# Performance work log

Hardware: AMD Instinct MI355X
Metric: run time of the kernel (lower is better)

The kernel has to match this reference:

```python
import jax, jax.numpy as jnp
import numpy as np
from jax import lax

B, C_IN, L = 32, 64, 8192
PF = 128


def caudil_conv(x, W, kw, dilation, causal_padding=0):
    """x: (B, C, L); W: (O, kw*C) with layout W[o, c*kw + j] (channel-major).
    Equivalent to the per-timestep sliced-Linear loop: VALID dilated conv."""
    C = x.shape[1]
    if causal_padding:
        x = jnp.pad(x, ((0, 0), (0, 0), (causal_padding, 0)))
    K = W.reshape(-1, C, kw)  # (O, C, kw)
    return lax.conv_general_dilated(
        x, K, window_strides=(1,), padding='VALID', rhs_dilation=(dilation,),
        dimension_numbers=('NCH', 'OIH', 'NCH'))


def setup_inputs() -> dict:
    key = jax.random.key(0)
    ks = jax.random.split(key, 10)
    s = lambda k, shp: (jax.random.normal(k, shp, dtype=jnp.float32) * 0.05)
    return {
        'x': jax.random.normal(ks[0], (B, C_IN, L), dtype=jnp.float32),
        'w7_1': s(ks[1], (6, 3 * C_IN)),
        'w7_3': s(ks[2], (PF, 3 * 6)),
        'w10_1': s(ks[3], (6, 3 * C_IN)),
        'w10_3': s(ks[4], (6, 3 * 6)),
        'w10_5': s(ks[5], (PF, 2 * 6)),
        'w15_1': s(ks[6], (6, 3 * C_IN)),
        'w15_3': s(ks[7], (6, 3 * 6)),
        'w15_5': s(ks[8], (PF, 3 * 6)),
    }


def reference(x, w7_1, w7_3, w10_1, w10_3, w10_5, w15_1, w15_3, w15_5):
    relu = jax.nn.relu
    # branch 7: (3,d1) -> (3,d2)
    m7 = relu(caudil_conv(x, w7_1, 3, 1))
    m7 = relu(caudil_conv(m7, w7_3, 3, 2))
    # branch 10: (3,d1) -> (3,d2) -> (2,d4,pad4)
    m10 = relu(caudil_conv(x, w10_1, 3, 1))
    m10 = relu(caudil_conv(m10, w10_3, 3, 2))
    m10 = relu(caudil_conv(m10, w10_5, 2, 4, causal_padding=4))
    # branch 15: (3,d1) -> (3,d2) -> (3,d4,pad8)
    m15 = relu(caudil_conv(x, w15_1, 3, 1))
    m15 = relu(caudil_conv(m15, w15_3, 3, 2))
    m15 = relu(caudil_conv(m15, w15_5, 3, 4, causal_padding=8))
    return jnp.concatenate([m7, m10, m15], axis=1)  # (B, 3*PF, L-6)
```

## Files before the change

kernel.cpp:

```cpp
#include <hip/hip_runtime.h>

constexpr int Bn   = 32;
constexpr int CIN  = 64;
constexpr int Lx   = 8192;
constexpr int L1   = 8190;
constexpr int LOUT = 8186;
constexpr int NCH  = 384;

constexpr int TB = 256;
constexpr int TT = 256;
constexpr int NTILES = (LOUT + TT - 1) / TT;

constexpr int W7v   = TT + 4;
constexpr int W10Av = TT + 8;
constexpr int W15Av = TT + 12;
constexpr int W10Bv = TT + 4;
constexpr int W15Bv = TT + 8;

__global__ void prep_weights(const float* __restrict__ w7_1,
                             const float* __restrict__ w10_1,
                             const float* __restrict__ w15_1,
                             float* __restrict__ ws) {
    int idx = blockIdx.x * blockDim.x + threadIdx.x;
    if (idx >= 64 * 54) return;
    int ci = idx / 54, r = idx % 54;
    int k = r / 3, j = r % 3;
    const float* src = (k < 6) ? w7_1 : ((k < 12) ? w10_1 : w15_1);
    int kk = (k < 6) ? k : ((k < 12) ? k - 6 : k - 12);
    ws[ci * 64 + r] = src[kk * 192 + ci * 3 + j];
}

__device__ __forceinline__ void store4(float* __restrict__ op, int t,
                                       float a0, float a1, float a2, float a3) {
    a0 = fmaxf(a0, 0.f); a1 = fmaxf(a1, 0.f);
    a2 = fmaxf(a2, 0.f); a3 = fmaxf(a3, 0.f);
    if (t + 3 < LOUT) {
        *(float2*)(op + t)     = make_float2(a0, a1);
        *(float2*)(op + t + 2) = make_float2(a2, a3);
    } else {
        if (t     < LOUT) op[t]     = a0;
        if (t + 1 < LOUT) op[t + 1] = a1;
        if (t + 2 < LOUT) op[t + 2] = a2;
        if (t + 3 < LOUT) op[t + 3] = a3;
    }
}

__global__ __launch_bounds__(TB)
void fused_inception(const float* __restrict__ x,
                     const float* __restrict__ wS1,
                     const float* __restrict__ w7_3,
                     const float* __restrict__ w10_3,
                     const float* __restrict__ w10_5,
                     const float* __restrict__ w15_3,
                     const float* __restrict__ w15_5,
                     float* __restrict__ out) {
    __shared__ float h7  [6 * W7v];
    __shared__ float h10a[6 * W10Av];
    __shared__ float h15a[6 * W15Av];
    __shared__ float h10b[6 * W10Bv];
    __shared__ float h15b[6 * W15Bv];

    const int tid  = threadIdx.x;
    const int tile = blockIdx.x;
    const int b    = blockIdx.y;
    const int t0   = tile * TT;
    const float* xb = x + (size_t)b * CIN * Lx;

    for (int p = tid; p < TT + 12; p += TB) {
        const int s = t0 - 8 + p;
        float acc[18];
        #pragma unroll
        for (int k = 0; k < 18; ++k) acc[k] = 0.f;
        if (s >= 0 && s < L1) {
            const float* xr = xb + s;
            for (int ci = 0; ci < CIN; ++ci) {
                const float x0 = xr[ci * Lx];
                const float x1 = xr[ci * Lx + 1];
                const float x2 = xr[ci * Lx + 2];
                const float* wr = wS1 + ci * 64;
                #pragma unroll
                for (int k = 0; k < 18; ++k) {
                    acc[k] = fmaf(wr[k * 3 + 0], x0, acc[k]);
                    acc[k] = fmaf(wr[k * 3 + 1], x1, acc[k]);
                    acc[k] = fmaf(wr[k * 3 + 2], x2, acc[k]);
                }
            }
            #pragma unroll
            for (int k = 0; k < 18; ++k) acc[k] = fmaxf(acc[k], 0.f);
        }
        if (p >= 8) {
            #pragma unroll
            for (int c = 0; c < 6; ++c) h7[c * W7v + (p - 8)] = acc[c];
        }
        if (p >= 4) {
            #pragma unroll
            for (int c = 0; c < 6; ++c) h10a[c * W10Av + (p - 4)] = acc[6 + c];
        }
        #pragma unroll
        for (int c = 0; c < 6; ++c) h15a[c * W15Av + p] = acc[12 + c];
    }
    __syncthreads();

    for (int p = tid; p < W10Bv; p += TB) {
        const int u = t0 - 4 + p;
        float v[18];
        #pragma unroll
        for (int c = 0; c < 6; ++c)
            #pragma unroll
            for (int j = 0; j < 3; ++j)
                v[c * 3 + j] = h10a[c * W10Av + p + 2 * j];
        #pragma unroll
        for (int k = 0; k < 6; ++k) {
            float a = 0.f;
            #pragma unroll
            for (int r = 0; r < 18; ++r) a = fmaf(w10_3[k * 18 + r], v[r], a);
            h10b[k * W10Bv + p] = (u >= 0) ? fmaxf(a, 0.f) : 0.f;
        }
    }
    for (int p = tid; p < W15Bv; p += TB) {
        const int u = t0 - 8 + p;
        float v[18];
        #pragma unroll
        for (int c = 0; c < 6; ++c)
            #pragma unroll
            for (int j = 0; j < 3; ++j)
                v[c * 3 + j] = h15a[c * W15Av + p + 2 * j];
        #pragma unroll
        for (int k = 0; k < 6; ++k) {
            float a = 0.f;
            #pragma unroll
            for (int r = 0; r < 18; ++r) a = fmaf(w15_3[k * 18 + r], v[r], a);
            h15b[k * W15Bv + p] = (u >= 0) ? fmaxf(a, 0.f) : 0.f;
        }
    }
    __syncthreads();

    const int tq = tid & 63;
    const int wv = tid >> 6;
    const int tt = tq * 4;
    const int tglob = t0 + tt;

    {
        float v[6][8];
        #pragma unroll
        for (int c = 0; c < 6; ++c) {
            float4 A = *(const float4*)&h7[c * W7v + tt];
            float4 Bv = *(const float4*)&h7[c * W7v + tt + 4];
            v[c][0] = A.x; v[c][1] = A.y; v[c][2] = A.z; v[c][3] = A.w;
            v[c][4] = Bv.x; v[c][5] = Bv.y; v[c][6] = Bv.z; v[c][7] = Bv.w;
        }
        for (int oi = 0; oi < 32; ++oi) {
            const int oc = wv * 32 + oi;
            const float* wr = w7_3 + oc * 18;
            float a0 = 0, a1 = 0, a2 = 0, a3 = 0;
            #pragma unroll
            for (int c = 0; c < 6; ++c)
                #pragma unroll
                for (int j = 0; j < 3; ++j) {
                    const float w = wr[c * 3 + j];
                    a0 = fmaf(w, v[c][0 + 2 * j], a0);
                    a1 = fmaf(w, v[c][1 + 2 * j], a1);
                    a2 = fmaf(w, v[c][2 + 2 * j], a2);
                    a3 = fmaf(w, v[c][3 + 2 * j], a3);
                }
            float* op = out + ((size_t)b * NCH + oc) * LOUT;
            store4(op, tglob, a0, a1, a2, a3);
        }
    }
    {
        float v[6][8];
        #pragma unroll
        for (int c = 0; c < 6; ++c) {
            float4 A = *(const float4*)&h10b[c * W10Bv + tt];
            float4 Bv = *(const float4*)&h10b[c * W10Bv + tt + 4];
            v[c][0] = A.x; v[c][1] = A.y; v[c][2] = A.z; v[c][3] = A.w;
            v[c][4] = Bv.x; v[c][5] = Bv.y; v[c][6] = Bv.z; v[c][7] = Bv.w;
        }
        for (int oi = 0; oi < 32; ++oi) {
            const int oc = wv * 32 + oi;
            const float* wr = w10_5 + oc * 12;
            float a0 = 0, a1 = 0, a2 = 0, a3 = 0;
            #pragma unroll
            for (int c = 0; c < 6; ++c) {
                const float w0 = wr[c * 2 + 0];
                const float w1 = wr[c * 2 + 1];
                a0 = fmaf(w0, v[c][0], a0); a0 = fmaf(w1, v[c][4], a0);
                a1 = fmaf(w0, v[c][1], a1); a1 = fmaf(w1, v[c][5], a1);
                a2 = fmaf(w0, v[c][2], a2); a2 = fmaf(w1, v[c][6], a2);
                a3 = fmaf(w0, v[c][3], a3); a3 = fmaf(w1, v[c][7], a3);
            }
            float* op = out + ((size_t)b * NCH + 128 + oc) * LOUT;
            store4(op, tglob, a0, a1, a2, a3);
        }
    }
    {
        float v[6][12];
        #pragma unroll
        for (int c = 0; c < 6; ++c) {
            float4 A = *(const float4*)&h15b[c * W15Bv + tt];
            float4 Bv = *(const float4*)&h15b[c * W15Bv + tt + 4];
            float4 Cv = *(const float4*)&h15b[c * W15Bv + tt + 8];
            v[c][0] = A.x;  v[c][1] = A.y;  v[c][2] = A.z;  v[c][3] = A.w;
            v[c][4] = Bv.x; v[c][5] = Bv.y; v[c][6] = Bv.z; v[c][7] = Bv.w;
            v[c][8] = Cv.x; v[c][9] = Cv.y; v[c][10] = Cv.z; v[c][11] = Cv.w;
        }
        for (int oi = 0; oi < 32; ++oi) {
            const int oc = wv * 32 + oi;
            const float* wr = w15_5 + oc * 18;
            float a0 = 0, a1 = 0, a2 = 0, a3 = 0;
            #pragma unroll
            for (int c = 0; c < 6; ++c)
                #pragma unroll
                for (int j = 0; j < 3; ++j) {
                    const float w = wr[c * 3 + j];
                    a0 = fmaf(w, v[c][0 + 4 * j], a0);
                    a1 = fmaf(w, v[c][1 + 4 * j], a1);
                    a2 = fmaf(w, v[c][2 + 4 * j], a2);
                    a3 = fmaf(w, v[c][3 + 4 * j], a3);
                }
            float* op = out + ((size_t)b * NCH + 256 + oc) * LOUT;
            store4(op, tglob, a0, a1, a2, a3);
        }
    }
}

extern "C" void kernel_launch(void* const* d_in, const int* in_sizes, int n_in,
                              void* d_out, int out_size, void* d_ws, size_t ws_size,
                              hipStream_t stream) {
    const float* x     = (const float*)d_in[0];
    const float* w7_1  = (const float*)d_in[1];
    const float* w7_3  = (const float*)d_in[2];
    const float* w10_1 = (const float*)d_in[3];
    const float* w10_3 = (const float*)d_in[4];
    const float* w10_5 = (const float*)d_in[5];
    const float* w15_1 = (const float*)d_in[6];
    const float* w15_3 = (const float*)d_in[7];
    const float* w15_5 = (const float*)d_in[8];
    float* out = (float*)d_out;
    float* ws  = (float*)d_ws;

    prep_weights<<<dim3(14), dim3(256), 0, stream>>>(w7_1, w10_1, w15_1, ws);
    fused_inception<<<dim3(NTILES, Bn), dim3(TB), 0, stream>>>(
        x, ws, w7_3, w10_3, w10_5, w15_3, w15_5, out);
}
```

Measured before the change: 523.5 us.

## Split fused inception kernel into per-branch blocks with one output per thread

Each block now handles a single branch (7, 10 or 15), adding a grid dimension of 3, so the per-block stage-1 work drops from 18 to 6 channels and shared memory shrinks. The final layer switches from 4 timesteps per thread over 32 channels to one timestep per thread over all 128 channels, giving fully coalesced scalar stores, and launch bounds request 8 blocks per CU. The aim is more parallelism and occupancy. The cost is that x is read from global memory three times, once per branch, instead of once.

```diff
diff --git a/kernel.cpp b/kernel.cpp
--- a/kernel.cpp
+++ b/kernel.cpp
@@ -10,12 +10,6 @@
 constexpr int TB = 256;
 constexpr int TT = 256;
 constexpr int NTILES = (LOUT + TT - 1) / TT;
-
-constexpr int W7v   = TT + 4;
-constexpr int W10Av = TT + 8;
-constexpr int W15Av = TT + 12;
-constexpr int W10Bv = TT + 4;
-constexpr int W15Bv = TT + 8;
 
 __global__ void prep_weights(const float* __restrict__ w7_1,
                              const float* __restrict__ w10_1,
@@ -30,22 +24,107 @@
     ws[ci * 64 + r] = src[kk * 192 + ci * 3 + j];
 }
 
-__device__ __forceinline__ void store4(float* __restrict__ op, int t,
-                                       float a0, float a1, float a2, float a3) {
-    a0 = fmaxf(a0, 0.f); a1 = fmaxf(a1, 0.f);
-    a2 = fmaxf(a2, 0.f); a3 = fmaxf(a3, 0.f);
-    if (t + 3 < LOUT) {
-        *(float2*)(op + t)     = make_float2(a0, a1);
-        *(float2*)(op + t + 2) = make_float2(a2, a3);
+template <int BR>
+__device__ __forceinline__ void run_branch(
+    float* __restrict__ smem,
+    const float* __restrict__ xb,
+    const float* __restrict__ wS1,
+    const float* __restrict__ wmid,
+    const float* __restrict__ wlast,
+    float* __restrict__ outb,
+    int t0)
+{
+    constexpr int PRE = (BR == 0) ? 0 : (BR == 1 ? 4 : 8);
+    constexpr int NA  = TT + 4 + PRE;
+    constexpr int NB  = NA - 4;
+    float* ha = smem;
+    float* hb = smem + 6 * NA;
+    const int tid = threadIdx.x;
+
+    for (int p = tid; p < NA; p += TB) {
+        const int s = t0 - PRE + p;
+        float a[6];
+        #pragma unroll
+        for (int c = 0; c < 6; ++c) a[c] = 0.f;
+        if (s >= 0 && s < L1) {
+            const float* xr = xb + s;
+            const float* wr = wS1 + BR * 18;
+            for (int ci = 0; ci < CIN; ++ci) {
+                const float x0 = xr[0];
+                const float x1 = xr[1];
+                const float x2 = xr[2];
+                #pragma unroll
+                for (int c = 0; c < 6; ++c) {
+                    a[c] = fmaf(wr[c * 3 + 0], x0, a[c]);
+                    a[c] = fmaf(wr[c * 3 + 1], x1, a[c]);
+                    a[c] = fmaf(wr[c * 3 + 2], x2, a[c]);
+                }
+                xr += Lx;
+                wr += 64;
+            }
+            #pragma unroll
+            for (int c = 0; c < 6; ++c) a[c] = fmaxf(a[c], 0.f);
+        }
+        #pragma unroll
+        for (int c = 0; c < 6; ++c) ha[c * NA + p] = a[c];
+    }
+    __syncthreads();
+
+    if (BR != 0) {
+        for (int q = tid; q < NB; q += TB) {
+            const int u = t0 - PRE + q;
+            float v[18];
+            #pragma unroll
+            for (int c = 0; c < 6; ++c)
+                #pragma unroll
+                for (int j = 0; j < 3; ++j)
+                    v[c * 3 + j] = ha[c * NA + q + 2 * j];
+            #pragma unroll
+            for (int k = 0; k < 6; ++k) {
+                float acc = 0.f;
+                #pragma unroll
+                for (int r = 0; r < 18; ++r)
+                    acc = fmaf(wmid[k * 18 + r], v[r], acc);
+                hb[k * NB + q] = (u >= 0) ? fmaxf(acc, 0.f) : 0.f;
+            }
+        }
+    }
+    __syncthreads();
+
+    const int t = t0 + tid;
+    const bool ok = (t < LOUT);
+    constexpr int NW = (BR == 1) ? 12 : 18;
+    float v[NW];
+    if (BR == 0) {
+        #pragma unroll
+        for (int c = 0; c < 6; ++c)
+            #pragma unroll
+            for (int j = 0; j < 3; ++j)
+                v[c * 3 + j] = ha[c * NA + tid + 2 * j];
+    } else if (BR == 1) {
+        #pragma unroll
+        for (int c = 0; c < 6; ++c)
+            #pragma unroll
+            for (int j = 0; j < 2; ++j)
+                v[c * 2 + j] = hb[c * NB + tid + 4 * j];
     } else {
-        if (t     < LOUT) op[t]     = a0;
-        if (t + 1 < LOUT) op[t + 1] = a1;
-        if (t + 2 < LOUT) op[t + 2] = a2;
-        if (t + 3 < LOUT) op[t + 3] = a3;
+        #pragma unroll
+        for (int c = 0; c < 6; ++c)
+            #pragma unroll
+            for (int j = 0; j < 3; ++j)
+                v[c * 3 + j] = hb[c * NB + tid + 4 * j];
+    }
+    #pragma unroll 4
+    for (int oc = 0; oc < 128; ++oc) {
+        const float* wp = wlast + oc * NW;
+        float acc = 0.f;
+        #pragma unroll
+        for (int r = 0; r < NW; ++r) acc = fmaf(wp[r], v[r], acc);
+        if (ok) outb[(size_t)oc * LOUT + t] = fmaxf(acc, 0.f);
     }
 }
 
-__global__ __launch_bounds__(TB)
+__global__ __launch_bounds__(TB, 8)
 void fused_inception(const float* __restrict__ x,
                      const float* __restrict__ wS1,
                      const float* __restrict__ w7_3,
@@ -54,174 +133,17 @@
                      const float* __restrict__ w15_3,
                      const float* __restrict__ w15_5,
                      float* __restrict__ out) {
-    __shared__ float h7  [6 * W7v];
-    __shared__ float h10a[6 * W10Av];
-    __shared__ float h15a[6 * W15Av];
-    __shared__ float h10b[6 * W10Bv];
-    __shared__ float h15b[6 * W15Bv];
-
-    const int tid  = threadIdx.x;
+    __shared__ float smem[6 * 268 + 6 * 264];
     const int tile = blockIdx.x;
-    const int b    = blockIdx.y;
+    const int br   = blockIdx.y;
+    const int b    = blockIdx.z;
     const int t0   = tile * TT;
     const float* xb = x + (size_t)b * CIN * Lx;
+    float* outb = out + ((size_t)b * NCH + (size_t)br * 128) * LOUT;
 
-    for (int p = tid; p < TT + 12; p += TB) {
-        const int s = t0 - 8 + p;
-        float acc[18];
-        #pragma unroll
-        for (int k = 0; k < 18; ++k) acc[k] = 0.f;
-        if (s >= 0 && s < L1) {
-            const float* xr = xb + s;
-            for (int ci = 0; ci < CIN; ++ci) {
-                const float x0 = xr[ci * Lx];
-                const float x1 = xr[ci * Lx + 1];
-                const float x2 = xr[ci * Lx + 2];
-                const float* wr = wS1 + ci * 64;
-                #pragma unroll
-                for (int k = 0; k < 18; ++k) {
-                    acc[k] = fmaf(wr[k * 3 + 0], x0, acc[k]);
-                    acc[k] = fmaf(wr[k * 3 + 1], x1, acc[k]);
-                    acc[k] = fmaf(wr[k * 3 + 2], x2, acc[k]);
-                }
-            }
-            #pragma unroll
-            for (int k = 0; k < 18; ++k) acc[k] = fmaxf(acc[k], 0.f);
-        }
-        if (p >= 8) {
-            #pragma unroll
-            for (int c = 0; c < 6; ++c) h7[c * W7v + (p - 8)] = acc[c];
-        }
-        if (p >= 4) {
-            #pragma unroll
-            for (int c = 0; c < 6; ++c) h10a[c * W10Av + (p - 4)] = acc[6 + c];
-        }
-        #pragma unroll
-        for (int c = 0; c < 6; ++c) h15a[c * W15Av + p] = acc[12 + c];
-    }
-    __syncthreads();
-
-    for (int p = tid; p < W10Bv; p += TB) {
-        const int u = t0 - 4 + p;
-        float v[18];
-        #pragma unroll
-        for (int c = 0; c < 6; ++c)
-            #pragma unroll
-            for (int j = 0; j < 3; ++j)
-                v[c * 3 + j] = h10a[c * W10Av + p + 2 * j];
-        #pragma unroll
-        for (int k = 0; k < 6; ++k) {
-            float a = 0.f;
-            #pragma unroll
-            for (int r = 0; r < 18; ++r) a = fmaf(w10_3[k * 18 + r], v[r], a);
-            h10b[k * W10Bv + p] = (u >= 0) ? fmaxf(a, 0.f) : 0.f;
-        }
-    }
-    for (int p = tid; p < W15Bv; p += TB) {
-        const int u = t0 - 8 + p;
-        float v[18];
-        #pragma unroll
-        for (int c = 0; c < 6; ++c)
-            #pragma unroll
-            for (int j = 0; j < 3; ++j)
-                v[c * 3 + j] = h15a[c * W15Av + p + 2 * j];
-        #pragma unroll
-        for (int k = 0; k < 6; ++k) {
-            float a = 0.f;
-            #pragma unroll
-            for (int r = 0; r < 18; ++r) a = fmaf(w15_3[k * 18 + r], v[r], a);
-            h15b[k * W15Bv + p] = (u >= 0) ? fmaxf(a, 0.f) : 0.f;
-        }
-    }
-    __syncthreads();
-
-    const int tq = tid & 63;
-    const int wv = tid >> 6;
-    const int tt = tq * 4;
-    const int tglob = t0 + tt;
-
-    {
-        float v[6][8];
-        #pragma unroll
-        for (int c = 0; c < 6; ++c) {
-            float4 A = *(const float4*)&h7[c * W7v + tt];
-            float4 Bv = *(const float4*)&h7[c * W7v + tt + 4];
-            v[c][0] = A.x; v[c][1] = A.y; v[c][2] = A.z; v[c][3] = A.w;
-            v[c][4] = Bv.x; v[c][5] = Bv.y; v[c][6] = Bv.z; v[c][7] = Bv.w;
-        }
-        for (int oi = 0; oi < 32; ++oi) {
-            const int oc = wv * 32 + oi;
-            const float* wr = w7_3 + oc * 18;
-            float a0 = 0, a1 = 0, a2 = 0, a3 = 0;
-            #pragma unroll
-            for (int c = 0; c < 6; ++c)
-                #pragma unroll
-                for (int j = 0; j < 3; ++j) {
-                    const float w = wr[c * 3 + j];
-                    a0 = fmaf(w, v[c][0 + 2 * j], a0);
-                    a1 = fmaf(w, v[c][1 + 2 * j], a1);
-                    a2 = fmaf(w, v[c][2 + 2 * j], a2);
-                    a3 = fmaf(w, v[c][3 + 2 * j], a3);
-                }
-            float* op = out + ((size_t)b * NCH + oc) * LOUT;
-            store4(op, tglob, a0, a1, a2, a3);
-        }
-    }
-    {
-        float v[6][8];
-        #pragma unroll
-        for (int c = 0; c < 6; ++c) {
-            float4 A = *(const float4*)&h10b[c * W10Bv + tt];
-            float4 Bv = *(const float4*)&h10b[c * W10Bv + tt + 4];
-            v[c][0] = A.x; v[c][1] = A.y; v[c][2] = A.z; v[c][3] = A.w;
-            v[c][4] = Bv.x; v[c][5] = Bv.y; v[c][6] = Bv.z; v[c][7] = Bv.w;
-        }
-        for (int oi = 0; oi < 32; ++oi) {
-            const int oc = wv * 32 + oi;
-            const float* wr = w10_5 + oc * 12;
-            float a0 = 0, a1 = 0, a2 = 0, a3 = 0;
-            #pragma unroll
-            for (int c = 0; c < 6; ++c) {
-                const float w0 = wr[c * 2 + 0];
-                const float w1 = wr[c * 2 + 1];
-                a0 = fmaf(w0, v[c][0], a0); a0 = fmaf(w1, v[c][4], a0);
-                a1 = fmaf(w0, v[c][1], a1); a1 = fmaf(w1, v[c][5], a1);
-                a2 = fmaf(w0, v[c][2], a2); a2 = fmaf(w1, v[c][6], a2);
-                a3 = fmaf(w0, v[c][3], a3); a3 = fmaf(w1, v[c][7], a3);
-            }
-            float* op = out + ((size_t)b * NCH + 128 + oc) * LOUT;
-            store4(op, tglob, a0, a1, a2, a3);
-        }
-    }
-    {
-        float v[6][12];
-        #pragma unroll
-        for (int c = 0; c < 6; ++c) {
-            float4 A = *(const float4*)&h15b[c * W15Bv + tt];
-            float4 Bv = *(const float4*)&h15b[c * W15Bv + tt + 4];
-            float4 Cv = *(const float4*)&h15b[c * W15Bv + tt + 8];
-            v[c][0] = A.x;  v[c][1] = A.y;  v[c][2] = A.z;  v[c][3] = A.w;
-            v[c][4] = Bv.x; v[c][5] = Bv.y; v[c][6] = Bv.z; v[c][7] = Bv.w;
-            v[c][8] = Cv.x; v[c][9] = Cv.y; v[c][10] = Cv.z; v[c][11] = Cv.w;
-        }
-        for (int oi = 0; oi < 32; ++oi) {
-            const int oc = wv * 32 + oi;
-            const float* wr = w15_5 + oc * 18;
-            float a0 = 0, a1 = 0, a2 = 0, a3 = 0;
-            #pragma unroll
-            for (int c = 0; c < 6; ++c)
-                #pragma unroll
-                for (int j = 0; j < 3; ++j) {
-                    const float w = wr[c * 3 + j];
-                    a0 = fmaf(w, v[c][0 + 4 * j], a0);
-                    a1 = fmaf(w, v[c][1 + 4 * j], a1);
-                    a2 = fmaf(w, v[c][2 + 4 * j], a2);
-                    a3 = fmaf(w, v[c][3 + 4 * j], a3);
-                }
-            float* op = out + ((size_t)b * NCH + 256 + oc) * LOUT;
-            store4(op, tglob, a0, a1, a2, a3);
-        }
-    }
+    if (br == 0)      run_branch<0>(smem, xb, wS1, nullptr, w7_3,  outb, t0);
+    else if (br == 1) run_branch<1>(smem, xb, wS1, w10_3,  w10_5, outb, t0);
+    else              run_branch<2>(smem, xb, wS1, w15_3,  w15_5, outb, t0);
 }
 
 extern "C" void kernel_launch(void* const* d_in, const int* in_sizes, int n_in,
@@ -240,6 +162,6 @@
     float* ws  = (float*)d_ws;
 
     prep_weights<<<dim3(14), dim3(256), 0, stream>>>(w7_1, w10_1, w15_1, ws);
-    fused_inception<<<dim3(NTILES, Bn), dim3(TB), 0, stream>>>(
+    fused_inception<<<dim3(NTILES, 3, Bn), dim3(TB), 0, stream>>>(
         x, ws, w7_3, w10_3, w10_5, w15_3, w15_5, out);
 }
```

Result: slower. 573.4 us (+9.5%).

## Double block size, split stage-1 channels across halves, use nontemporal stores

Applied to the files above, without the earlier changes.

Block size goes from 256 to 512 threads. The first conv stage splits its 18 output channels into two halves of 9, one per half of the block, and the two second-stage branches run concurrently on separate halves. The final pointwise stage now has each thread produce 2 timesteps instead of 4, with float2 nontemporal stores to the output. The aim is to shorten the long serial first-stage loop per thread and cut register pressure, at the cost of reloading x in both halves and issuing narrower stores.

```diff
diff --git a/kernel.cpp b/kernel.cpp
--- a/kernel.cpp
+++ b/kernel.cpp
@@ -7,7 +7,7 @@
 constexpr int LOUT = 8186;
 constexpr int NCH  = 384;
 
-constexpr int TB = 256;
+constexpr int TB = 512;
 constexpr int TT = 256;
 constexpr int NTILES = (LOUT + TT - 1) / TT;
 
@@ -16,6 +16,9 @@
 constexpr int W15Av = TT + 12;
 constexpr int W10Bv = TT + 4;
 constexpr int W15Bv = TT + 8;
+constexpr int NA_MAX = TT + 12;
+
+typedef float v2f __attribute__((ext_vector_type(2)));
 
 __global__ void prep_weights(const float* __restrict__ w7_1,
                              const float* __restrict__ w10_1,
@@ -30,22 +33,18 @@
     ws[ci * 64 + r] = src[kk * 192 + ci * 3 + j];
 }
 
-__device__ __forceinline__ void store4(float* __restrict__ op, int t,
-                                       float a0, float a1, float a2, float a3) {
+__device__ __forceinline__ void store2(float* __restrict__ op, int t,
+                                       float a0, float a1) {
     a0 = fmaxf(a0, 0.f); a1 = fmaxf(a1, 0.f);
-    a2 = fmaxf(a2, 0.f); a3 = fmaxf(a3, 0.f);
-    if (t + 3 < LOUT) {
-        *(float2*)(op + t)     = make_float2(a0, a1);
-        *(float2*)(op + t + 2) = make_float2(a2, a3);
-    } else {
-        if (t     < LOUT) op[t]     = a0;
-        if (t + 1 < LOUT) op[t + 1] = a1;
-        if (t + 2 < LOUT) op[t + 2] = a2;
-        if (t + 3 < LOUT) op[t + 3] = a3;
-    }
-}
-
-__global__ __launch_bounds__(TB)
+    if (t + 1 < LOUT) {
+        v2f v2; v2.x = a0; v2.y = a1;
+        __builtin_nontemporal_store(v2, (v2f*)(op + t));
+    } else if (t < LOUT) {
+        __builtin_nontemporal_store(a0, op + t);
+    }
+}
+
+__global__ __launch_bounds__(TB, 8)
 void fused_inception(const float* __restrict__ x,
                      const float* __restrict__ wS1,
                      const float* __restrict__ w7_3,
@@ -66,93 +65,112 @@
     const int t0   = tile * TT;
     const float* xb = x + (size_t)b * CIN * Lx;
 
-    for (int p = tid; p < TT + 12; p += TB) {
-        const int s = t0 - 8 + p;
-        float acc[18];
-        #pragma unroll
-        for (int k = 0; k < 18; ++k) acc[k] = 0.f;
-        if (s >= 0 && s < L1) {
-            const float* xr = xb + s;
-            for (int ci = 0; ci < CIN; ++ci) {
-                const float x0 = xr[ci * Lx];
-                const float x1 = xr[ci * Lx + 1];
-                const float x2 = xr[ci * Lx + 2];
-                const float* wr = wS1 + ci * 64;
-                #pragma unroll
-                for (int k = 0; k < 18; ++k) {
-                    acc[k] = fmaf(wr[k * 3 + 0], x0, acc[k]);
-                    acc[k] = fmaf(wr[k * 3 + 1], x1, acc[k]);
-                    acc[k] = fmaf(wr[k * 3 + 2], x2, acc[k]);
-                }
-            }
-            #pragma unroll
-            for (int k = 0; k < 18; ++k) acc[k] = fmaxf(acc[k], 0.f);
-        }
-        if (p >= 8) {
-            #pragma unroll
-            for (int c = 0; c < 6; ++c) h7[c * W7v + (p - 8)] = acc[c];
-        }
-        if (p >= 4) {
-            #pragma unroll
-            for (int c = 0; c < 6; ++c) h10a[c * W10Av + (p - 4)] = acc[6 + c];
-        }
-        #pragma unroll
-        for (int c = 0; c < 6; ++c) h15a[c * W15Av + p] = acc[12 + c];
+    {
+        const int half = tid >> 8;
+        const int q    = tid & 255;
+        for (int p = q; p < NA_MAX; p += 256) {
+            const int s = t0 - 8 + p;
+            float a[9];
+            #pragma unroll
+            for (int k = 0; k < 9; ++k) a[k] = 0.f;
+            if (s >= 0 && s < L1) {
+                const float* xr = xb + s;
+                const float* wr = wS1 + half * 27;
+                for (int ci = 0; ci < CIN; ++ci) {
+                    const float x0 = xr[0];
+                    const float x1 = xr[1];
+                    const float x2 = xr[2];
+                    #pragma unroll
+                    for (int k = 0; k < 9; ++k) {
+                        a[k] = fmaf(wr[k * 3 + 0], x0, a[k]);
+                        a[k] = fmaf(wr[k * 3 + 1], x1, a[k]);
+                        a[k] = fmaf(wr[k * 3 + 2], x2, a[k]);
+                    }
+                    xr += Lx;
+                    wr += 64;
+                }
+                #pragma unroll
+                for (int k = 0; k < 9; ++k) a[k] = fmaxf(a[k], 0.f);
+            }
+            if (half == 0) {
+                if (p >= 8) {
+                    #pragma unroll
+                    for (int c = 0; c < 6; ++c) h7[c * W7v + (p - 8)] = a[c];
+                }
+                if (p >= 4) {
+                    #pragma unroll
+                    for (int c = 0; c < 3; ++c) h10a[c * W10Av + (p - 4)] = a[6 + c];
+                }
+            } else {
+                if (p >= 4) {
+                    #pragma unroll
+                    for (int c = 0; c < 3; ++c) h10a[(3 + c) * W10Av + (p - 4)] = a[c];
+                }
+                #pragma unroll
+                for (int c = 0; c < 6; ++c) h15a[c * W15Av + p] = a[3 + c];
+            }
+        }
     }
     __syncthreads();
 
-    for (int p = tid; p < W10Bv; p += TB) {
-        const int u = t0 - 4 + p;
-        float v[18];
-        #pragma unroll
-        for (int c = 0; c < 6; ++c)
-            #pragma unroll
-            for (int j = 0; j < 3; ++j)
-                v[c * 3 + j] = h10a[c * W10Av + p + 2 * j];
-        #pragma unroll
-        for (int k = 0; k < 6; ++k) {
-            float a = 0.f;
-            #pragma unroll
-            for (int r = 0; r < 18; ++r) a = fmaf(w10_3[k * 18 + r], v[r], a);
-            h10b[k * W10Bv + p] = (u >= 0) ? fmaxf(a, 0.f) : 0.f;
-        }
-    }
-    for (int p = tid; p < W15Bv; p += TB) {
-        const int u = t0 - 8 + p;
-        float v[18];
-        #pragma unroll
-        for (int c = 0; c < 6; ++c)
-            #pragma unroll
-            for (int j = 0; j < 3; ++j)
-                v[c * 3 + j] = h15a[c * W15Av + p + 2 * j];
-        #pragma unroll
-        for (int k = 0; k < 6; ++k) {
-            float a = 0.f;
-            #pragma unroll
-            for (int r = 0; r < 18; ++r) a = fmaf(w15_3[k * 18 + r], v[r], a);
-            h15b[k * W15Bv + p] = (u >= 0) ? fmaxf(a, 0.f) : 0.f;
+    if (tid < 256) {
+        for (int p = tid; p < W10Bv; p += 256) {
+            const int u = t0 - 4 + p;
+            float v[18];
+            #pragma unroll
+            for (int c = 0; c < 6; ++c)
+                #pragma unroll
+                for (int j = 0; j < 3; ++j)
+                    v[c * 3 + j] = h10a[c * W10Av + p + 2 * j];
+            #pragma unroll
+            for (int k = 0; k < 6; ++k) {
+                float acc = 0.f;
+                #pragma unroll
+                for (int r = 0; r < 18; ++r)
+                    acc = fmaf(w10_3[k * 18 + r], v[r], acc);
+                h10b[k * W10Bv + p] = (u >= 0) ? fmaxf(acc, 0.f) : 0.f;
+            }
+        }
+    } else {
+        for (int p = tid - 256; p < W15Bv; p += 256) {
+            const int u = t0 - 8 + p;
+            float v[18];
+            #pragma unroll
+            for (int c = 0; c < 6; ++c)
+                #pragma unroll
+                for (int j = 0; j < 3; ++j)
+                    v[c * 3 + j] = h15a[c * W15Av + p + 2 * j];
+            #pragma unroll
+            for (int k = 0; k < 6; ++k) {
+                float acc = 0.f;
+                #pragma unroll
+                for (int r = 0; r < 18; ++r)
+                    acc = fmaf(w15_3[k * 18 + r], v[r], acc);
+                h15b[k * W15Bv + p] = (u >= 0) ? fmaxf(acc, 0.f) : 0.f;
+            }
         }
     }
     __syncthreads();
 
-    const int tq = tid & 63;
-    const int wv = tid >> 6;
-    const int tt = tq * 4;
+    const int tq = tid & 127;
+    const int wv = tid >> 7;
+    const int tt = tq * 2;
     const int tglob = t0 + tt;
 
     {
-        float v[6][8];
+        float v[6][6];
         #pragma unroll
         for (int c = 0; c < 6; ++c) {
-            float4 A = *(const float4*)&h7[c * W7v + tt];
-            float4 Bv = *(const float4*)&h7[c * W7v + tt + 4];
-            v[c][0] = A.x; v[c][1] = A.y; v[c][2] = A.z; v[c][3] = A.w;
-            v[c][4] = Bv.x; v[c][5] = Bv.y; v[c][6] = Bv.z; v[c][7] = Bv.w;
+            float2 A = *(const float2*)&h7[c * W7v + tt];
+            float2 Bv = *(const float2*)&h7[c * W7v + tt + 2];
+            float2 Cv = *(const float2*)&h7[c * W7v + tt + 4];
+            v[c][0] = A.x; v[c][1] = A.y; v[c][2] = Bv.x;
+            v[c][3] = Bv.y; v[c][4] = Cv.x; v[c][5] = Cv.y;
         }
         for (int oi = 0; oi < 32; ++oi) {
             const int oc = wv * 32 + oi;
             const float* wr = w7_3 + oc * 18;
-            float a0 = 0, a1 = 0, a2 = 0, a3 = 0;
+            float a0 = 0, a1 = 0;
             #pragma unroll
             for (int c = 0; c < 6; ++c)
                 #pragma unroll
@@ -160,66 +178,58 @@
                     const float w = wr[c * 3 + j];
                     a0 = fmaf(w, v[c][0 + 2 * j], a0);
                     a1 = fmaf(w, v[c][1 + 2 * j], a1);
-                    a2 = fmaf(w, v[c][2 + 2 * j], a2);
-                    a3 = fmaf(w, v[c][3 + 2 * j], a3);
                 }
             float* op = out + ((size_t)b * NCH + oc) * LOUT;
-            store4(op, tglob, a0, a1, a2, a3);
-        }
-    }
-    {
-        float v[6][8];
+            store2(op, tglob, a0, a1);
+        }
+    }
+    {
+        float v[6][4];
         #pragma unroll
         for (int c = 0; c < 6; ++c) {
-            float4 A = *(const float4*)&h10b[c * W10Bv + tt];
-            float4 Bv = *(const float4*)&h10b[c * W10Bv + tt + 4];
-            v[c][0] = A.x; v[c][1] = A.y; v[c][2] = A.z; v[c][3] = A.w;
-            v[c][4] = Bv.x; v[c][5] = Bv.y; v[c][6] = Bv.z; v[c][7] = Bv.w;
+            float2 A = *(const float2*)&h10b[c * W10Bv + tt];
+            float2 Bv = *(const float2*)&h10b[c * W10Bv + tt + 4];
+            v[c][0] = A.x; v[c][1] = A.y; v[c][2] = Bv.x; v[c][3] = Bv.y;
         }
         for (int oi = 0; oi < 32; ++oi) {
             const int oc = wv * 32 + oi;
             const float* wr = w10_5 + oc * 12;
-            float a0 = 0, a1 = 0, a2 = 0, a3 = 0;
+            float a0 = 0, a1 = 0;
             #pragma unroll
             for (int c = 0; c < 6; ++c) {
                 const float w0 = wr[c * 2 + 0];
                 const float w1 = wr[c * 2 + 1];
-                a0 = fmaf(w0, v[c][0], a0); a0 = fmaf(w1, v[c][4], a0);
-                a1 = fmaf(w0, v[c][1], a1); a1 = fmaf(w1, v[c][5], a1);
-                a2 = fmaf(w0, v[c][2], a2); a2 = fmaf(w1, v[c][6], a2);
-                a3 = fmaf(w0, v[c][3], a3); a3 = fmaf(w1, v[c][7], a3);
+                a0 = fmaf(w0, v[c][0], a0); a0 = fmaf(w1, v[c][2], a0);
+                a1 = fmaf(w0, v[c][1], a1); a1 = fmaf(w1, v[c][3], a1);
             }
             float* op = out + ((size_t)b * NCH + 128 + oc) * LOUT;
-            store4(op, tglob, a0, a1, a2, a3);
-        }
-    }
-    {
-        float v[6][12];
+            store2(op, tglob, a0, a1);
+        }
+    }
+    {
+        float v[6][6];
         #pragma unroll
         for (int c = 0; c < 6; ++c) {
-            float4 A = *(const float4*)&h15b[c * W15Bv + tt];
-            float4 Bv = *(const float4*)&h15b[c * W15Bv + tt + 4];
-            float4 Cv = *(const float4*)&h15b[c * W15Bv + tt + 8];
-            v[c][0] = A.x;  v[c][1] = A.y;  v[c][2] = A.z;  v[c][3] = A.w;
-            v[c][4] = Bv.x; v[c][5] = Bv.y; v[c][6] = Bv.z; v[c][7] = Bv.w;
-            v[c][8] = Cv.x; v[c][9] = Cv.y; v[c][10] = Cv.z; v[c][11] = Cv.w;
+            float2 A = *(const float2*)&h15b[c * W15Bv + tt];
+            float2 Bv = *(const float2*)&h15b[c * W15Bv + tt + 4];
+            float2 Cv = *(const float2*)&h15b[c * W15Bv + tt + 8];
+            v[c][0] = A.x; v[c][1] = A.y; v[c][2] = Bv.x;
+            v[c][3] = Bv.y; v[c][4] = Cv.x; v[c][5] = Cv.y;
         }
         for (int oi = 0; oi < 32; ++oi) {
             const int oc = wv * 32 + oi;
             const float* wr = w15_5 + oc * 18;
-            float a0 = 0, a1 = 0, a2 = 0, a3 = 0;
+            float a0 = 0, a1 = 0;
             #pragma unroll
             for (int c = 0; c < 6; ++c)
                 #pragma unroll
                 for (int j = 0; j < 3; ++j) {
                     const float w = wr[c * 3 + j];
-                    a0 = fmaf(w, v[c][0 + 4 * j], a0);
-                    a1 = fmaf(w, v[c][1 + 4 * j], a1);
-                    a2 = fmaf(w, v[c][2 + 4 * j], a2);
-                    a3 = fmaf(w, v[c][3 + 4 * j], a3);
+                    a0 = fmaf(w, v[c][0 + 2 * j], a0);
+                    a1 = fmaf(w, v[c][1 + 2 * j], a1);
                 }
             float* op = out + ((size_t)b * NCH + 256 + oc) * LOUT;
-            store4(op, tglob, a0, a1, a2, a3);
+            store2(op, tglob, a0, a1);
         }
     }
 }
```

Result: slower. 733.2 us (+40.0%).
